# Performance work log

Measured on AMD Instinct MI355X. Metric: run time of the kernel, lower is better.

The kernel has to match this reference:

```python
import jax, jax.numpy as jnp
import numpy as np

N, D, P, NS = 2048, 64, 32, 512  # nnodes, stop_embedding_size, preference_dim, n_active_stops
LEAKY_SLOPE = 0.01
COS_EPS = 1e-8


def setup_inputs() -> dict:
    key = jax.random.key(0)
    ks = jax.random.split(key, 10)
    dist = jax.random.uniform(ks[0], (N, N), dtype=jnp.float32)
    stops = jax.random.randint(ks[1], (NS,), 0, N)
    emb_w = jax.random.normal(ks[2], (N, D), dtype=jnp.float32) * 0.05      # nn.Embedding weight
    lin_l_w = jax.random.normal(ks[3], (P, D), dtype=jnp.float32) * 0.05    # SAGEConv lin_l (aggregated)
    lin_l_b = jnp.zeros((P,), dtype=jnp.float32)
    lin_r_w = jax.random.normal(ks[4], (P, D), dtype=jnp.float32) * 0.05    # SAGEConv lin_r (root)
    edge_w = jax.random.normal(ks[5], (2 * P,), dtype=jnp.float32) * 0.05   # edge_summarizer weight
    edge_b = jnp.zeros((), dtype=jnp.float32)
    in_len = 2 * N + 3 + P
    comb_w = jax.random.normal(ks[6], (N, in_len), dtype=jnp.float32) * 0.02  # combiner weight
    comb_b = jnp.zeros((N,), dtype=jnp.float32)
    return {
        "dist": dist, "emb_w": emb_w,
        "lin_l_w": lin_l_w, "lin_l_b": lin_l_b, "lin_r_w": lin_r_w,
        "edge_w": edge_w, "edge_b": edge_b,
        "comb_w": comb_w, "comb_b": comb_b,
        "stops": stops, "weekday": 3, "vehicles": 5,
    }


def reference(dist, emb_w, lin_l_w, lin_l_b, lin_r_w, edge_w, edge_b,
              comb_w, comb_b, stops, weekday, vehicles):
    dt = emb_w.dtype
    # --- cosine-similarity graph build ---
    norm = jnp.maximum(jnp.linalg.norm(emb_w, axis=1, keepdims=True), COS_EPS)
    xn = emb_w / norm
    sim = xn @ xn.T                                   # [N, N]
    sim = sim * (1.0 - jnp.eye(N, dtype=dt))          # fill_diagonal_(0)
    keep = jnp.zeros((N,), dtype=bool).at[stops].set(True)
    adj = ((sim > 0.5) & keep[:, None] & keep[None, :]).astype(dt)  # [N, N]
    # --- SAGEConv (mean aggregation): lin_l(mean_j x_j) + lin_r(x_i) ---
    deg = jnp.maximum(adj.sum(axis=1, keepdims=True), 1.0)
    agg = (adj @ emb_w) / deg                         # [N, D]
    pref = agg @ lin_l_w.T + lin_l_b + emb_w @ lin_r_w.T   # [N, P]
    # --- all-pairs edge summaries: Linear([pref_i, pref_j]) + LeakyReLU ---
    # equivalent to concat-then-linear, without materializing [N^2, 2P]
    a = pref @ edge_w[:P]                             # [N]
    b = pref @ edge_w[P:]                             # [N]
    es = a[:, None] + b[None, :] + edge_b             # [N, N]
    es = jnp.where(es >= 0, es, LEAKY_SLOPE * es)
    # --- combiner + log-softmax ---
    weekday_feat = jnp.full((N, 1), weekday, dtype=dt)
    vehicle_feat = jnp.full((N, 1), vehicles, dtype=dt)
    stop_feat = keep.astype(dt)[:, None]
    combined = jnp.concatenate([pref, es, dist, weekday_feat, vehicle_feat, stop_feat], axis=1)
    out = combined @ comb_w.T + comb_b                # [N, N]
    return jax.nn.log_softmax(out, axis=1)
```

## Files before the change

### kernel.cpp

```cpp
#include <hip/hip_runtime.h>

typedef unsigned short u16;
typedef __attribute__((ext_vector_type(8))) short bf16x8;
typedef __attribute__((ext_vector_type(4))) float f32x4;

__device__ __forceinline__ u16 f2bf(float f) {
    return (u16)((__float_as_uint(f) + 0x8000u) >> 16);
}

#define N_NODES 2048
#define D_EMB 64
#define P_DIM 32
#define NS_STOPS 512
#define IN_LEN 4131
#define NKT 65

#define SWZ(row, c) ((((row) * 8) + ((c) ^ ((row) & 7))) * 8)

__device__ __forceinline__ void gload16(const u16* g, u16* l) {
    __builtin_amdgcn_global_load_lds((const __attribute__((address_space(1))) void*)g,
                                     (__attribute__((address_space(3))) void*)l, 16, 0, 0);
}

__global__ __launch_bounds__(256) void k_aggpref(const float* __restrict__ emb, const int* __restrict__ stops,
                                                 const float* __restrict__ lin_l_w, const float* __restrict__ lin_l_b,
                                                 const float* __restrict__ lin_r_w, const float* __restrict__ edge_w,
                                                 float* __restrict__ pref, float* __restrict__ av, float* __restrict__ bv) {
    int i = blockIdx.x, t = threadIdx.x;
    __shared__ int bm[64];
    __shared__ int kl[NS_STOPS];
    __shared__ int cnt, degL;
    __shared__ float xi[D_EMB];
    __shared__ float aggL[D_EMB];
    __shared__ float niS;
    if (t < 64) bm[t] = 0;
    if (t == 0) { cnt = 0; degL = 0; }
    if (t < D_EMB) { xi[t] = emb[i * D_EMB + t]; aggL[t] = 0.f; }
    __syncthreads();
    {
        int s0 = stops[t], s1 = stops[t + 256];
        atomicOr(&bm[s0 >> 5], 1 << (s0 & 31));
        atomicOr(&bm[s1 >> 5], 1 << (s1 & 31));
    }
    __syncthreads();
    {
        int w = bm[t >> 2];
        int base = (t >> 2) * 32 + (t & 3) * 8;
        #pragma unroll
        for (int e = 0; e < 8; ++e)
            if ((w >> ((t & 3) * 8 + e)) & 1) { int p = atomicAdd(&cnt, 1); kl[p] = base + e; }
    }
    if (t < 64) {
        float s = xi[t] * xi[t];
        #pragma unroll
        for (int off = 32; off; off >>= 1) s += __shfl_xor(s, off, 64);
        if (t == 0) niS = fmaxf(sqrtf(s), 1e-8f);
    }
    __syncthreads();
    int ki = (bm[i >> 5] >> (i & 31)) & 1;
    if (ki) {
        int nk = cnt;
        float ni = niS;
        const f32x4* xiv = (const f32x4*)xi;
        for (int u = t; u < nk; u += 256) {
            int j = kl[u];
            if (j == i) continue;
            const f32x4* ej = (const f32x4*)&emb[j * D_EMB];
            f32x4 er[16];
            f32x4 dv = {0.f, 0.f, 0.f, 0.f};
            f32x4 sv = {0.f, 0.f, 0.f, 0.f};
            #pragma unroll
            for (int d = 0; d < 16; ++d) {
                er[d] = ej[d];
                dv += xiv[d] * er[d];
                sv += er[d] * er[d];
            }
            float dot = dv[0] + dv[1] + dv[2] + dv[3];
            float nj = fmaxf(sqrtf(sv[0] + sv[1] + sv[2] + sv[3]), 1e-8f);
            if (dot > 0.5f * ni * nj) {
                atomicAdd(&degL, 1);
                #pragma unroll
                for (int d = 0; d < 16; ++d) {
                    atomicAdd(&aggL[d * 4 + 0], er[d][0]);
                    atomicAdd(&aggL[d * 4 + 1], er[d][1]);
                    atomicAdd(&aggL[d * 4 + 2], er[d][2]);
                    atomicAdd(&aggL[d * 4 + 3], er[d][3]);
                }
            }
        }
    }
    __syncthreads();
    if (t < D_EMB) {
        float deg = fmaxf((float)degL, 1.0f);
        aggL[t] = ki ? (aggL[t] / deg) : 0.f;
    }
    __syncthreads();
    if (t < P_DIM) {
        float s = lin_l_b[t];
        const float* wl = &lin_l_w[t * D_EMB];
        const float* wr = &lin_r_w[t * D_EMB];
        #pragma unroll
        for (int d = 0; d < D_EMB; ++d) s += aggL[d] * wl[d] + xi[d] * wr[d];
        pref[i * P_DIM + t] = s;
        float a = s * edge_w[t];
        float b = s * edge_w[P_DIM + t];
        #pragma unroll
        for (int off = 16; off; off >>= 1) { a += __shfl_xor(a, off, 64); b += __shfl_xor(b, off, 64); }
        if (t == 0) { av[i] = a; bv[i] = b; }
    }
}

__global__ __launch_bounds__(256) void k_pack(const float* __restrict__ comb_w, const float* __restrict__ comb_b,
                                              const int* __restrict__ wk_p, const int* __restrict__ vh_p,
                                              const float* __restrict__ dist, const float* __restrict__ pref,
                                              const float* __restrict__ av, const float* __restrict__ bv,
                                              const float* __restrict__ edge_b,
                                              u16* __restrict__ Bp, u16* __restrict__ Ap,
                                              float* __restrict__ cvec, float* __restrict__ w3) {
    int bid = blockIdx.x, t = threadIdx.x;
    if (bid < 2048) {
        int j = bid;
        int nt = j >> 7, r = j & 127;
        const float* cw = comb_w + (size_t)j * IN_LEN;
        for (int q = t; q < 520; q += 256) {
            int kt = q >> 3, c = q & 7;
            int k0 = q * 8;
            bf16x8 v;
            if (k0 < 4096) {
                f32x4 f0, f1;
                __builtin_memcpy(&f0, cw + 32 + k0, 16);
                __builtin_memcpy(&f1, cw + 36 + k0, 16);
                #pragma unroll
                for (int e = 0; e < 4; ++e) { v[e] = (short)f2bf(f0[e]); v[4 + e] = (short)f2bf(f1[e]); }
            } else if (k0 < 4128) {
                f32x4 f0, f1;
                __builtin_memcpy(&f0, cw + (k0 - 4096), 16);
                __builtin_memcpy(&f1, cw + (k0 - 4092), 16);
                #pragma unroll
                for (int e = 0; e < 4; ++e) { v[e] = (short)f2bf(f0[e]); v[4 + e] = (short)f2bf(f1[e]); }
            } else {
                #pragma unroll
                for (int e = 0; e < 8; ++e) v[e] = 0;
            }
            size_t off = (((size_t)nt * NKT + kt) * 128 + r) * 64 + (size_t)((c ^ (r & 7)) * 8);
            *(bf16x8*)&Bp[off] = v;
        }
        if (t == 0) {
            float wk = (float)wk_p[0], vh = (float)vh_p[0];
            cvec[j] = wk * cw[4128] + vh * cw[4129] + comb_b[j];
            w3[j] = cw[4130];
        }
    } else {
        int row = bid - 2048;
        int rt = row >> 6, r = row & 63;
        float ab = av[row] + edge_b[0];
        const float* drow = dist + (size_t)row * 2048;
        const float* prow = pref + (size_t)row * P_DIM;
        for (int q = t; q < 520; q += 256) {
            int kt = q >> 3, c = q & 7;
            int k0 = q * 8;
            bf16x8 v;
            if (k0 < 2048) {
                const f32x4* bp = (const f32x4*)(bv + k0);
                f32x4 f0 = bp[0], f1 = bp[1];
                #pragma unroll
                for (int e = 0; e < 4; ++e) {
                    float s0 = ab + f0[e]; s0 = (s0 >= 0.f) ? s0 : 0.01f * s0;
                    float s1 = ab + f1[e]; s1 = (s1 >= 0.f) ? s1 : 0.01f * s1;
                    v[e] = (short)f2bf(s0); v[4 + e] = (short)f2bf(s1);
                }
            } else if (k0 < 4096) {
                const f32x4* dp = (const f32x4*)(drow + (k0 - 2048));
                f32x4 f0 = dp[0], f1 = dp[1];
                #pragma unroll
                for (int e = 0; e < 4; ++e) { v[e] = (short)f2bf(f0[e]); v[4 + e] = (short)f2bf(f1[e]); }
            } else if (k0 < 4128) {
                const f32x4* pp = (const f32x4*)(prow + (k0 - 4096));
                f32x4 f0 = pp[0], f1 = pp[1];
                #pragma unroll
                for (int e = 0; e < 4; ++e) { v[e] = (short)f2bf(f0[e]); v[4 + e] = (short)f2bf(f1[e]); }
            } else {
                #pragma unroll
                for (int e = 0; e < 8; ++e) v[e] = 0;
            }
            size_t off = (((size_t)rt * NKT + kt) * 64 + r) * 64 + (size_t)((c ^ (r & 7)) * 8);
            *(bf16x8*)&Ap[off] = v;
        }
    }
}

__global__ __launch_bounds__(256) void k_gemm_d(const u16* __restrict__ Ap, const u16* __restrict__ Bp,
                                                float* __restrict__ Cout) {
    __shared__ __attribute__((aligned(16))) short As[2][64 * 64];
    __shared__ __attribute__((aligned(16))) short Bs[2][128 * 64];
    int t = threadIdx.x;
    int mt = blockIdx.y, nt = blockIdx.x;
    int tileM = mt * 64, tileN = nt * 128;
    int lane = t & 63;
    int wid = t >> 6;
    int waveM = wid & 1, waveN = wid >> 1;
    int l16 = lane & 15, quad = lane >> 4;

    f32x4 acc[2][4];
    #pragma unroll
    for (int a_ = 0; a_ < 2; ++a_)
        #pragma unroll
        for (int b_ = 0; b_ < 4; ++b_) acc[a_][b_] = (f32x4){0.f, 0.f, 0.f, 0.f};

    const u16* ga = Ap + ((size_t)mt * NKT) * 4096 + t * 8;
    const u16* gb = Bp + ((size_t)nt * NKT) * 8192 + t * 8;

    {
        u16* ad = (u16*)As[0] + t * 8;
        u16* bd = (u16*)Bs[0] + t * 8;
        gload16(ga, ad);
        gload16(ga + 2048, ad + 2048);
        #pragma unroll
        for (int u = 0; u < 4; ++u) gload16(gb + u * 2048, bd + u * 2048);
    }

    int cur = 0;
    for (int kt = 0; kt < NKT; ++kt) {
        __syncthreads();
        if (kt + 1 < NKT) {
            const u16* gan = ga + (size_t)(kt + 1) * 4096;
            const u16* gbn = gb + (size_t)(kt + 1) * 8192;
            u16* ad = (u16*)As[cur ^ 1] + t * 8;
            u16* bd = (u16*)Bs[cur ^ 1] + t * 8;
            gload16(gan, ad);
            gload16(gan + 2048, ad + 2048);
            #pragma unroll
            for (int u = 0; u < 4; ++u) gload16(gbn + u * 2048, bd + u * 2048);
        }
        const short* Asc = As[cur];
        const short* Bsc = Bs[cur];
        #pragma unroll
        for (int kk = 0; kk < 64; kk += 32) {
            int cbase = kk >> 3;
            bf16x8 af[2], bfr[4];
            #pragma unroll
            for (int mi = 0; mi < 2; ++mi) {
                int row = waveM * 32 + mi * 16 + l16;
                af[mi] = *(const bf16x8*)&Asc[SWZ(row, cbase + quad)];
            }
            #pragma unroll
            for (int ni = 0; ni < 4; ++ni) {
                int row = waveN * 64 + ni * 16 + l16;
                bfr[ni] = *(const bf16x8*)&Bsc[SWZ(row, cbase + quad)];
            }
            #pragma unroll
            for (int mi = 0; mi < 2; ++mi)
                #pragma unroll
                for (int ni = 0; ni < 4; ++ni)
                    acc[mi][ni] = __builtin_amdgcn_mfma_f32_16x16x32_bf16(af[mi], bfr[ni], acc[mi][ni], 0, 0, 0);
        }
        cur ^= 1;
    }
    #pragma unroll
    for (int mi = 0; mi < 2; ++mi)
        #pragma unroll
        for (int ni = 0; ni < 4; ++ni) {
            int row = tileM + waveM * 32 + mi * 16 + quad * 4;
            int col = tileN + waveN * 64 + ni * 16 + l16;
            float* cp = Cout + (size_t)row * N_NODES + col;
            #pragma unroll
            for (int rr = 0; rr < 4; ++rr) cp[(size_t)rr * N_NODES] = acc[mi][ni][rr];
        }
}

__global__ __launch_bounds__(256) void k_epi(const float* __restrict__ cvec, const float* __restrict__ w3,
                                             const int* __restrict__ stops, float* __restrict__ out) {
    int i = blockIdx.x, t = threadIdx.x;
    __shared__ int bm[64];
    __shared__ float redmax[4], redsum[4];
    if (t < 64) bm[t] = 0;
    __syncthreads();
    {
        int s0 = stops[t], s1 = stops[t + 256];
        atomicOr(&bm[s0 >> 5], 1 << (s0 & 31));
        atomicOr(&bm[s1 >> 5], 1 << (s1 & 31));
    }
    __syncthreads();
    float ki = (float)((bm[i >> 5] >> (i & 31)) & 1);
    f32x4* orow = (f32x4*)(out + (size_t)i * N_NODES);
    const f32x4* cv = (const f32x4*)cvec;
    const f32x4* wv = (const f32x4*)w3;
    f32x4 v0 = orow[t] + cv[t] + ki * wv[t];
    f32x4 v1 = orow[t + 256] + cv[t + 256] + ki * wv[t + 256];
    float vmax = fmaxf(fmaxf(fmaxf(v0[0], v0[1]), fmaxf(v0[2], v0[3])),
                       fmaxf(fmaxf(v1[0], v1[1]), fmaxf(v1[2], v1[3])));
    #pragma unroll
    for (int off = 32; off; off >>= 1) vmax = fmaxf(vmax, __shfl_xor(vmax, off, 64));
    if ((t & 63) == 0) redmax[t >> 6] = vmax;
    __syncthreads();
    vmax = fmaxf(fmaxf(redmax[0], redmax[1]), fmaxf(redmax[2], redmax[3]));
    float se = 0.f;
    #pragma unroll
    for (int e = 0; e < 4; ++e) se += expf(v0[e] - vmax) + expf(v1[e] - vmax);
    #pragma unroll
    for (int off = 32; off; off >>= 1) se += __shfl_xor(se, off, 64);
    if ((t & 63) == 0) redsum[t >> 6] = se;
    __syncthreads();
    se = redsum[0] + redsum[1] + redsum[2] + redsum[3];
    float lz = vmax + logf(se);
    orow[t] = v0 - lz;
    orow[t + 256] = v1 - lz;
}

extern "C" void kernel_launch(void* const* d_in, const int* in_sizes, int n_in,
                              void* d_out, int out_size, void* d_ws, size_t ws_size,
                              hipStream_t stream) {
    const float* dist    = (const float*)d_in[0];
    const float* emb     = (const float*)d_in[1];
    const float* lin_l_w = (const float*)d_in[2];
    const float* lin_l_b = (const float*)d_in[3];
    const float* lin_r_w = (const float*)d_in[4];
    const float* edge_w  = (const float*)d_in[5];
    const float* edge_b  = (const float*)d_in[6];
    const float* comb_w  = (const float*)d_in[7];
    const float* comb_b  = (const float*)d_in[8];
    const int* stops     = (const int*)d_in[9];
    const int* wk        = (const int*)d_in[10];
    const int* vh        = (const int*)d_in[11];

    char* ws = (char*)d_ws;
    float* pref  = (float*)(ws + 0);
    float* av    = (float*)(ws + 262144);
    float* bv    = (float*)(ws + 270336);
    float* cvec  = (float*)(ws + 278528);
    float* w3    = (float*)(ws + 286720);
    u16*   Ap    = (u16*)(ws + 294912);
    u16*   Bp    = (u16*)(ws + 17334272);
    float* out   = (float*)d_out;

    hipLaunchKernelGGL(k_aggpref, dim3(2048),   dim3(256), 0, stream, emb, stops,
                       lin_l_w, lin_l_b, lin_r_w, edge_w, pref, av, bv);
    hipLaunchKernelGGL(k_pack,    dim3(4096),   dim3(256), 0, stream, comb_w, comb_b, wk, vh,
                       dist, pref, av, bv, edge_b, Bp, Ap, cvec, w3);
    hipLaunchKernelGGL(k_gemm_d,  dim3(16, 32), dim3(256), 0, stream, Ap, Bp, out);
    hipLaunchKernelGGL(k_epi,     dim3(2048),   dim3(256), 0, stream, cvec, w3, stops, out);
}
```

Baseline: 193.4 us.

## Triple-buffer GEMM LDS loads with vmcnt waits and retile pack kernel by k-tile

The GEMM moves from double to triple buffering in LDS. Loads are issued two k-tiles ahead, and a partial s_waitcnt vmcnt(6) replaces a full sync before each tile, so more memory latency can overlap with MFMA work. Separately, the pack kernel is regridded so each block writes one contiguous 64-wide k-tile of the packed A/B layout, which makes the stores contiguous but the reads from comb_w and dist strided. Triple buffering raises LDS use to 72KB per block, which may lower occupancy.

```diff
diff --git a/kernel.cpp b/kernel.cpp
--- a/kernel.cpp
+++ b/kernel.cpp
@@ -117,14 +117,19 @@
                                               const float* __restrict__ edge_b,
                                               u16* __restrict__ Bp, u16* __restrict__ Ap,
                                               float* __restrict__ cvec, float* __restrict__ w3) {
-    int bid = blockIdx.x, t = threadIdx.x;
-    if (bid < 2048) {
-        int j = bid;
-        int nt = j >> 7, r = j & 127;
-        const float* cw = comb_w + (size_t)j * IN_LEN;
-        for (int q = t; q < 520; q += 256) {
-            int kt = q >> 3, c = q & 7;
-            int k0 = q * 8;
+    int kt = blockIdx.x;
+    int ty = blockIdx.y;
+    int t = threadIdx.x;
+    if (ty < 16) {
+        int nt = ty;
+        u16* tb = Bp + ((size_t)nt * NKT + kt) * 8192;
+        #pragma unroll
+        for (int it = 0; it < 4; ++it) {
+            int q = t + it * 256;
+            int r = q >> 3, c = q & 7;
+            int j = nt * 128 + r;
+            int k0 = kt * 64 + c * 8;
+            const float* cw = comb_w + (size_t)j * IN_LEN;
             bf16x8 v;
             if (k0 < 4096) {
                 f32x4 f0, f1;
@@ -142,27 +147,30 @@
                 #pragma unroll
                 for (int e = 0; e < 8; ++e) v[e] = 0;
             }
-            size_t off = (((size_t)nt * NKT + kt) * 128 + r) * 64 + (size_t)((c ^ (r & 7)) * 8);
-            *(bf16x8*)&Bp[off] = v;
-        }
-        if (t == 0) {
+            *(bf16x8*)&tb[r * 64 + ((c ^ (r & 7)) * 8)] = v;
+        }
+        if (kt == 64 && t < 128) {
+            int j = nt * 128 + t;
+            const float* cw = comb_w + (size_t)j * IN_LEN;
             float wk = (float)wk_p[0], vh = (float)vh_p[0];
             cvec[j] = wk * cw[4128] + vh * cw[4129] + comb_b[j];
             w3[j] = cw[4130];
         }
     } else {
-        int row = bid - 2048;
-        int rt = row >> 6, r = row & 63;
-        float ab = av[row] + edge_b[0];
-        const float* drow = dist + (size_t)row * 2048;
-        const float* prow = pref + (size_t)row * P_DIM;
-        for (int q = t; q < 520; q += 256) {
-            int kt = q >> 3, c = q & 7;
-            int k0 = q * 8;
+        int rt = ty - 16;
+        u16* ta = Ap + ((size_t)rt * NKT + kt) * 4096;
+        float eb = edge_b[0];
+        #pragma unroll
+        for (int it = 0; it < 2; ++it) {
+            int q = t + it * 256;
+            int r = q >> 3, c = q & 7;
+            int row = rt * 64 + r;
+            int k0 = kt * 64 + c * 8;
             bf16x8 v;
             if (k0 < 2048) {
-                const f32x4* bp = (const f32x4*)(bv + k0);
-                f32x4 f0 = bp[0], f1 = bp[1];
+                float ab = av[row] + eb;
+                f32x4 f0 = *(const f32x4*)(bv + k0);
+                f32x4 f1 = *(const f32x4*)(bv + k0 + 4);
                 #pragma unroll
                 for (int e = 0; e < 4; ++e) {
                     float s0 = ab + f0[e]; s0 = (s0 >= 0.f) ? s0 : 0.01f * s0;
@@ -170,12 +178,12 @@
                     v[e] = (short)f2bf(s0); v[4 + e] = (short)f2bf(s1);
                 }
             } else if (k0 < 4096) {
-                const f32x4* dp = (const f32x4*)(drow + (k0 - 2048));
+                const f32x4* dp = (const f32x4*)(dist + (size_t)row * 2048 + (k0 - 2048));
                 f32x4 f0 = dp[0], f1 = dp[1];
                 #pragma unroll
                 for (int e = 0; e < 4; ++e) { v[e] = (short)f2bf(f0[e]); v[4 + e] = (short)f2bf(f1[e]); }
             } else if (k0 < 4128) {
-                const f32x4* pp = (const f32x4*)(prow + (k0 - 4096));
+                const f32x4* pp = (const f32x4*)(pref + (size_t)row * P_DIM + (k0 - 4096));
                 f32x4 f0 = pp[0], f1 = pp[1];
                 #pragma unroll
                 for (int e = 0; e < 4; ++e) { v[e] = (short)f2bf(f0[e]); v[4 + e] = (short)f2bf(f1[e]); }
@@ -183,16 +191,15 @@
                 #pragma unroll
                 for (int e = 0; e < 8; ++e) v[e] = 0;
             }
-            size_t off = (((size_t)rt * NKT + kt) * 64 + r) * 64 + (size_t)((c ^ (r & 7)) * 8);
-            *(bf16x8*)&Ap[off] = v;
+            *(bf16x8*)&ta[r * 64 + ((c ^ (r & 7)) * 8)] = v;
         }
     }
 }
 
 __global__ __launch_bounds__(256) void k_gemm_d(const u16* __restrict__ Ap, const u16* __restrict__ Bp,
                                                 float* __restrict__ Cout) {
-    __shared__ __attribute__((aligned(16))) short As[2][64 * 64];
-    __shared__ __attribute__((aligned(16))) short Bs[2][128 * 64];
+    __shared__ __attribute__((aligned(16))) short As[3][64 * 64];
+    __shared__ __attribute__((aligned(16))) short Bs[3][128 * 64];
     int t = threadIdx.x;
     int mt = blockIdx.y, nt = blockIdx.x;
     int tileM = mt * 64, tileN = nt * 128;
@@ -210,27 +217,32 @@
     const u16* ga = Ap + ((size_t)mt * NKT) * 4096 + t * 8;
     const u16* gb = Bp + ((size_t)nt * NKT) * 8192 + t * 8;
 
-    {
-        u16* ad = (u16*)As[0] + t * 8;
-        u16* bd = (u16*)Bs[0] + t * 8;
-        gload16(ga, ad);
-        gload16(ga + 2048, ad + 2048);
-        #pragma unroll
-        for (int u = 0; u < 4; ++u) gload16(gb + u * 2048, bd + u * 2048);
-    }
+#define ISSUE(ktv, bb) do { \
+        const u16* gan = ga + (size_t)(ktv) * 4096; \
+        const u16* gbn = gb + (size_t)(ktv) * 8192; \
+        u16* ad = (u16*)As[bb] + t * 8; \
+        u16* bd = (u16*)Bs[bb] + t * 8; \
+        gload16(gan, ad); \
+        gload16(gan + 2048, ad + 2048); \
+        gload16(gbn, bd); \
+        gload16(gbn + 2048, bd + 2048); \
+        gload16(gbn + 4096, bd + 4096); \
+        gload16(gbn + 6144, bd + 6144); \
+    } while (0)
+
+    ISSUE(0, 0);
+    ISSUE(1, 1);
 
     int cur = 0;
     for (int kt = 0; kt < NKT; ++kt) {
-        __syncthreads();
-        if (kt + 1 < NKT) {
-            const u16* gan = ga + (size_t)(kt + 1) * 4096;
-            const u16* gbn = gb + (size_t)(kt + 1) * 8192;
-            u16* ad = (u16*)As[cur ^ 1] + t * 8;
-            u16* bd = (u16*)Bs[cur ^ 1] + t * 8;
-            gload16(gan, ad);
-            gload16(gan + 2048, ad + 2048);
-            #pragma unroll
-            for (int u = 0; u < 4; ++u) gload16(gbn + u * 2048, bd + u * 2048);
+        if (kt < NKT - 1) asm volatile("s_waitcnt vmcnt(6)" ::: "memory");
+        else              asm volatile("s_waitcnt vmcnt(0)" ::: "memory");
+        __builtin_amdgcn_sched_barrier(0);
+        __builtin_amdgcn_s_barrier();
+        __builtin_amdgcn_sched_barrier(0);
+        if (kt + 2 < NKT) {
+            int b2 = cur + 2; if (b2 >= 3) b2 -= 3;
+            ISSUE(kt + 2, b2);
         }
         const short* Asc = As[cur];
         const short* Bsc = Bs[cur];
@@ -254,8 +266,9 @@
                 for (int ni = 0; ni < 4; ++ni)
                     acc[mi][ni] = __builtin_amdgcn_mfma_f32_16x16x32_bf16(af[mi], bfr[ni], acc[mi][ni], 0, 0, 0);
         }
-        cur ^= 1;
-    }
+        cur = cur + 1; if (cur >= 3) cur = 0;
+    }
+#undef ISSUE
     #pragma unroll
     for (int mi = 0; mi < 2; ++mi)
         #pragma unroll
@@ -335,7 +348,7 @@
 
     hipLaunchKernelGGL(k_aggpref, dim3(2048),   dim3(256), 0, stream, emb, stops,
                        lin_l_w, lin_l_b, lin_r_w, edge_w, pref, av, bv);
-    hipLaunchKernelGGL(k_pack,    dim3(4096),   dim3(256), 0, stream, comb_w, comb_b, wk, vh,
+    hipLaunchKernelGGL(k_pack,    dim3(65, 48), dim3(256), 0, stream, comb_w, comb_b, wk, vh,
                        dist, pref, av, bv, edge_b, Bp, Ap, cvec, w3);
     hipLaunchKernelGGL(k_gemm_d,  dim3(16, 32), dim3(256), 0, stream, Ap, Bp, out);
     hipLaunchKernelGGL(k_epi,     dim3(2048),   dim3(256), 0, stream, cvec, w3, stops, out);
```

Measured after the change: 198.4 us. +2.6%, slower.
